# Performance work log

Measured on AMD Instinct MI355X. Metric: run time of the kernel, lower is better.

## Reference

```python
import jax, jax.numpy as jnp
import numpy as np

N_EMBD = 1024
N_HEAD = 16
STRIDE = 128
C = 8
SEQ = 2048
BATCH = 2


def _sparse_causal_mask(nd, ns, stride, c, dtype):
    # Faithful vectorization of _sparse_attention_mask:
    # column j is globally visible if (j % stride) >= stride - c (the last c
    # columns of each stride block), each query also sees its own stride block,
    # and everything is causally masked (j <= q).
    j = jnp.arange(ns)
    q = jnp.arange(ns)[:, None]
    col_sel = (j % stride) >= (stride - c)          # strided summary columns
    same_block = (j[None, :] // stride) == (q // stride)  # local block
    causal = j[None, :] <= q
    mask = ((col_sel[None, :] | same_block) & causal).astype(dtype)
    return mask[ns - nd:]


def setup_inputs() -> dict:
    key = jax.random.key(0)
    k1, k2, k3 = jax.random.split(key, 3)
    inputs = jax.random.normal(k1, (BATCH, SEQ, N_EMBD), dtype=jnp.float32)
    w_attn = jax.random.normal(k2, (N_EMBD, 3 * N_EMBD), dtype=jnp.float32) * 0.02
    b_attn = jnp.zeros((3 * N_EMBD,), dtype=jnp.float32)
    proj_std = 0.02 / np.sqrt(2 * 24)  # n_layer = 24
    w_proj = jax.random.normal(k3, (N_EMBD, N_EMBD), dtype=jnp.float32) * proj_std
    b_proj = jnp.zeros((N_EMBD,), dtype=jnp.float32)
    return {"inputs": inputs, "w_attn": w_attn, "b_attn": b_attn,
            "w_proj": w_proj, "b_proj": b_proj}


def reference(inputs, w_attn, b_attn, w_proj, b_proj):
    B, S, E = inputs.shape
    H = N_HEAD
    D = E // H
    qkv = inputs @ w_attn + b_attn                     # [B,S,3E]
    q, k, v = jnp.split(qkv, 3, axis=-1)
    def split_heads(x):
        return x.reshape(B, S, H, D).transpose(0, 2, 1, 3)  # [B,H,S,D]
    q, k, v = split_heads(q), split_heads(k), split_heads(v)
    present = jnp.stack([k, v], axis=1)                # [B,2,H,S,D]
    scale = jnp.asarray(D, q.dtype) ** 0.5
    w = jnp.einsum('bhqd,bhkd->bhqk', q, k) / scale    # [B,H,S,S]
    mask = _sparse_causal_mask(S, S, STRIDE, C, w.dtype)
    w = w * mask - 1e10 * (1.0 - mask)
    p = jax.nn.softmax(w, axis=-1).astype(v.dtype)
    h = jnp.einsum('bhqk,bhkd->bhqd', p, v)            # [B,H,S,D]
    h = h.transpose(0, 2, 1, 3).reshape(B, S, E)       # merge heads
    h = h @ w_proj + b_proj
    # dropout p=0.0 (eval) -> identity
    return (h, present)
```

## Files before the change

### kernel.cpp

```cpp
#include <hip/hip_runtime.h>
#include <stdint.h>

typedef unsigned short u16;
typedef unsigned int u32;
typedef __attribute__((ext_vector_type(4))) float f32x4;
typedef __attribute__((ext_vector_type(4))) u16 u16x4;
typedef __attribute__((ext_vector_type(8))) __bf16 bf16x8;

__device__ __forceinline__ u16 f2bf(float f) {
  u32 u = __builtin_bit_cast(u32, f);
  u = (u + 0x7FFFu + ((u >> 16) & 1u)) >> 16;
  return (u16)u;
}

__device__ __forceinline__ void gload_lds16(const void* g, void* l) {
  __builtin_amdgcn_global_load_lds(
      (const __attribute__((address_space(1))) void*)(uintptr_t)(g),
      (__attribute__((address_space(3))) void*)(u32)(uintptr_t)(l),
      16, 0, 0);
}

__global__ void k_cvt(const float* __restrict__ in, u16* __restrict__ out, int n4) {
  int i = blockIdx.x * 256 + threadIdx.x;
  if (i >= n4) return;
  f32x4 v = ((const f32x4*)in)[i];
  u16x4 o = { f2bf(v.x), f2bf(v.y), f2bf(v.z), f2bf(v.w) };
  ((u16x4*)out)[i] = o;
}

__global__ void k_transpose(const float* __restrict__ in, u16* __restrict__ out,
                            int K, int N) {
  __shared__ float tile[32][33];
  int n0 = blockIdx.x * 32, k0 = blockIdx.y * 32;
  int t = threadIdx.x;
  int c = t & 31, r0 = t >> 5;
#pragma unroll
  for (int i = 0; i < 4; ++i)
    tile[r0 + i * 8][c] = in[(size_t)(k0 + r0 + i * 8) * N + n0 + c];
  __syncthreads();
  int on = t >> 3, ok = (t & 7) * 4;
  u16x4 o = { f2bf(tile[ok + 0][on]), f2bf(tile[ok + 1][on]),
              f2bf(tile[ok + 2][on]), f2bf(tile[ok + 3][on]) };
  *(u16x4*)&out[(size_t)(n0 + on) * K + k0 + ok] = o;
}

template <int EPI>
__global__ __launch_bounds__(256) void k_gemm(
    const u16* __restrict__ A, const u16* __restrict__ Bt,
    const float* __restrict__ bias, u16* __restrict__ outq,
    float* __restrict__ outp, int M, int N, int K) {
  __shared__ u16 a_lds[128 * 64];
  __shared__ u16 b_lds[128 * 64];
  const int t = threadIdx.x;
  const int lane = t & 63, w = t >> 6;
  const int m0 = blockIdx.y * 128, n0 = blockIdx.x * 128;
  const int srow = t >> 3;
  const int scb = (t & 7) * 16;
  const int ssw = scb ^ ((srow & 7) << 4);
  const size_t pitch = (size_t)K * 2;
  const char* aS = (const char*)A + (size_t)(m0 + srow) * pitch + ssw;
  const char* bS = (const char*)Bt + (size_t)(n0 + srow) * pitch + ssw;
  char* al = (char*)a_lds + t * 16;
  char* bl = (char*)b_lds + t * 16;
  const int wm = (w >> 1) * 64, wn = (w & 1) * 64;
  const int cc = lane & 15, g = lane >> 4;

  f32x4 acc[4][4] = {};

  for (int kt = 0; kt < K; kt += 64) {
    __syncthreads();
#pragma unroll
    for (int i = 0; i < 4; ++i) {
      gload_lds16(aS + (size_t)kt * 2 + (size_t)i * 32 * pitch, al + i * 4096);
      gload_lds16(bS + (size_t)kt * 2 + (size_t)i * 32 * pitch, bl + i * 4096);
    }
    __syncthreads();
#pragma unroll
    for (int kk = 0; kk < 2; ++kk) {
      bf16x8 af[4], bf_[4];
#pragma unroll
      for (int mf = 0; mf < 4; ++mf) {
        int row = wm + mf * 16 + cc;
        af[mf] = *(const bf16x8*)((const char*)a_lds + row * 128 +
                                  ((kk * 64 + g * 16) ^ ((row & 7) << 4)));
      }
#pragma unroll
      for (int nf = 0; nf < 4; ++nf) {
        int row = wn + nf * 16 + cc;
        bf_[nf] = *(const bf16x8*)((const char*)b_lds + row * 128 +
                                   ((kk * 64 + g * 16) ^ ((row & 7) << 4)));
      }
#pragma unroll
      for (int mf = 0; mf < 4; ++mf)
#pragma unroll
        for (int nf = 0; nf < 4; ++nf)
          acc[mf][nf] = __builtin_amdgcn_mfma_f32_16x16x32_bf16(
              af[mf], bf_[nf], acc[mf][nf], 0, 0, 0);
    }
  }

  float bv[4];
#pragma unroll
  for (int nf = 0; nf < 4; ++nf) bv[nf] = bias[n0 + wn + nf * 16 + cc];

#pragma unroll
  for (int mf = 0; mf < 4; ++mf)
#pragma unroll
    for (int nf = 0; nf < 4; ++nf) {
      int n = n0 + wn + nf * 16 + cc;
#pragma unroll
      for (int j = 0; j < 4; ++j) {
        int m = m0 + wm + mf * 16 + g * 4 + j;
        float v = acc[mf][nf][j] + bv[nf];
        if (EPI == 0) {
          if (n < 1024) {
            outq[(size_t)m * 1024 + n] = f2bf(v);
          } else {
            int nn = n - 1024;
            int kv = nn >> 10, n2 = nn & 1023;
            int bb = m >> 11, ss = m & 2047;
            outp[((((size_t)bb * 2 + kv) * 16 + (n2 >> 6)) * 2048 + ss) * 64 +
                 (n2 & 63)] = v;
          }
        } else {
          outp[(size_t)m * N + n] = v;
        }
      }
    }
}

__global__ __launch_bounds__(256) void k_attn(const u16* __restrict__ qws,
                                              const float* __restrict__ present,
                                              u16* __restrict__ hws) {
  const int qb = blockIdx.x, h = blockIdx.y, b = blockIdx.z;
  const int t = threadIdx.x, lane = t & 63, w = t >> 6;
  const int cc = lane & 15, g = lane >> 4;

  __shared__ u16 k_lds[256 * 72];
  __shared__ u16 q_lds[128 * 72];
  __shared__ u16 vt_lds[64 * 264];
  __shared__ u16 p_lds[4][32 * 136];
  __shared__ float rsum[4][32];

  const float* kbase = present + ((size_t)(b * 2 + 0) * 16 + h) * (2048 * 64);
  const float* vbase = present + ((size_t)(b * 2 + 1) * 16 + h) * (2048 * 64);

  {
    int seg = t & 15;
#pragma unroll
    for (int iter = 0; iter < 16; ++iter) {
      int r = (t >> 4) + iter * 16;
      int idx = r - 128;
      int gr = (r < 128) ? (qb * 128 + r) : ((idx >> 3) * 128 + 120 + (idx & 7));
      f32x4 v = *(const f32x4*)(kbase + (size_t)gr * 64 + seg * 4);
      u16x4 o = { f2bf(v.x), f2bf(v.y), f2bf(v.z), f2bf(v.w) };
      *(u16x4*)&k_lds[r * 72 + seg * 4] = o;
    }
  }
  {
    int seg = t & 15;
    int d0 = seg * 4;
#pragma unroll
    for (int iter = 0; iter < 4; ++iter) {
      int r0 = ((t >> 4) + iter * 16) * 4;
      f32x4 vv[4];
#pragma unroll
      for (int i = 0; i < 4; ++i) {
        int r = r0 + i;
        int idx = r - 128;
        int gr = (r < 128) ? (qb * 128 + r) : ((idx >> 3) * 128 + 120 + (idx & 7));
        vv[i] = *(const f32x4*)(vbase + (size_t)gr * 64 + d0);
      }
#pragma unroll
      for (int jd = 0; jd < 4; ++jd) {
        u16x4 o = { f2bf(vv[0][jd]), f2bf(vv[1][jd]),
                    f2bf(vv[2][jd]), f2bf(vv[3][jd]) };
        *(u16x4*)&vt_lds[(d0 + jd) * 264 + r0] = o;
      }
    }
  }
  {
    const char* qsrc = (const char*)qws +
        ((size_t)(b * 2048 + qb * 128 + (t >> 3)) * 1024 + (size_t)h * 64) * 2 +
        (t & 7) * 16;
#pragma unroll
    for (int iter = 0; iter < 4; ++iter) {
      int row = (t >> 3) + iter * 32;
      bf16x8 qv = *(const bf16x8*)(qsrc + (size_t)iter * 32 * 2048);
      *(bf16x8*)((char*)q_lds + row * 144 + (t & 7) * 16) = qv;
    }
  }
  __syncthreads();

  bf16x8 qf_[2][2];
#pragma unroll
  for (int qf = 0; qf < 2; ++qf)
#pragma unroll
    for (int kk = 0; kk < 2; ++kk)
      qf_[qf][kk] = *(const bf16x8*)((const char*)q_lds +
                                     (w * 32 + qf * 16 + cc) * 144 + kk * 64 + g * 16);

  f32x4 s[16][2] = {};
#pragma unroll
  for (int kf = 0; kf < 16; ++kf)
#pragma unroll
    for (int kk = 0; kk < 2; ++kk) {
      bf16x8 kfr = *(const bf16x8*)((const char*)k_lds +
                                    (kf * 16 + cc) * 144 + kk * 64 + g * 16);
#pragma unroll
      for (int qf = 0; qf < 2; ++qf)
        s[kf][qf] = __builtin_amdgcn_mfma_f32_16x16x32_bf16(kfr, qf_[qf][kk],
                                                            s[kf][qf], 0, 0, 0);
    }

  const int nsum = 128 + 8 * qb;
#pragma unroll
  for (int qf = 0; qf < 2; ++qf) {
    int q_local = w * 32 + qf * 16 + cc;
    float mx = -1e30f;
#pragma unroll
    for (int kf = 0; kf < 16; ++kf)
#pragma unroll
      for (int j = 0; j < 4; ++j) {
        int key = kf * 16 + g * 4 + j;
        float v = s[kf][qf][j] * 0.125f;
        bool vis = (key < 128) ? (key <= q_local) : (key < nsum);
        v = vis ? v : -1e30f;
        s[kf][qf][j] = v;
        mx = fmaxf(mx, v);
      }
    mx = fmaxf(mx, __shfl_xor(mx, 16));
    mx = fmaxf(mx, __shfl_xor(mx, 32));
    float sum = 0.f;
#pragma unroll
    for (int kf = 0; kf < 16; ++kf)
#pragma unroll
      for (int j = 0; j < 4; ++j) {
        float p = exp2f((s[kf][qf][j] - mx) * 1.44269504088896f);
        s[kf][qf][j] = p;
        sum += p;
      }
    sum += __shfl_xor(sum, 16);
    sum += __shfl_xor(sum, 32);
    if (g == 0) rsum[w][qf * 16 + cc] = sum;
  }

  f32x4 o_[2][4] = {};
#pragma unroll
  for (int ch = 0; ch < 2; ++ch) {
#pragma unroll
    for (int qf = 0; qf < 2; ++qf)
#pragma unroll
      for (int kf2 = 0; kf2 < 8; ++kf2) {
        int kf = ch * 8 + kf2;
        u16x4 o = { f2bf(s[kf][qf][0]), f2bf(s[kf][qf][1]),
                    f2bf(s[kf][qf][2]), f2bf(s[kf][qf][3]) };
        *(u16x4*)&p_lds[w][(qf * 16 + cc) * 136 + kf2 * 16 + g * 4] = o;
      }
#pragma unroll
    for (int kk = 0; kk < 4; ++kk) {
      bf16x8 pa[2], vb[4];
#pragma unroll
      for (int mf = 0; mf < 2; ++mf)
        pa[mf] = *(const bf16x8*)((const char*)p_lds[w] +
                                  (mf * 16 + cc) * 272 + kk * 64 + g * 16);
#pragma unroll
      for (int nf = 0; nf < 4; ++nf)
        vb[nf] = *(const bf16x8*)((const char*)vt_lds +
                                  (nf * 16 + cc) * 528 + (ch * 4 + kk) * 64 + g * 16);
#pragma unroll
      for (int mf = 0; mf < 2; ++mf)
#pragma unroll
        for (int nf = 0; nf < 4; ++nf)
          o_[mf][nf] = __builtin_amdgcn_mfma_f32_16x16x32_bf16(pa[mf], vb[nf],
                                                               o_[mf][nf], 0, 0, 0);
    }
  }

#pragma unroll
  for (int mf = 0; mf < 2; ++mf)
#pragma unroll
    for (int j = 0; j < 4; ++j) {
      float inv = 1.0f / rsum[w][mf * 16 + g * 4 + j];
      size_t row = (size_t)(b * 2048 + qb * 128 + w * 32 + mf * 16 + g * 4 + j);
#pragma unroll
      for (int nf = 0; nf < 4; ++nf)
        hws[row * 1024 + h * 64 + nf * 16 + cc] = f2bf(o_[mf][nf][j] * inv);
    }
}

extern "C" void kernel_launch(void* const* d_in, const int* in_sizes, int n_in,
                              void* d_out, int out_size, void* d_ws, size_t ws_size,
                              hipStream_t stream) {
  const float* x      = (const float*)d_in[0];
  const float* w_attn = (const float*)d_in[1];
  const float* b_attn = (const float*)d_in[2];
  const float* w_proj = (const float*)d_in[3];
  const float* b_proj = (const float*)d_in[4];
  float* h_out   = (float*)d_out;
  float* present = (float*)d_out + 4194304;

  char* ws = (char*)d_ws;
  u16* xbf = (u16*)(ws);
  u16* qws = (u16*)(ws + (8u << 20));
  u16* wat = (u16*)(ws + (16u << 20));
  u16* wpt = (u16*)(ws + (22u << 20));
  u16* hws = xbf;

  k_cvt<<<4096, 256, 0, stream>>>(x, xbf, 4096 * 1024 / 4);
  k_transpose<<<dim3(96, 32), 256, 0, stream>>>(w_attn, wat, 1024, 3072);
  k_transpose<<<dim3(32, 32), 256, 0, stream>>>(w_proj, wpt, 1024, 1024);
  k_gemm<0><<<dim3(24, 32), 256, 0, stream>>>(xbf, wat, b_attn, qws, present,
                                              4096, 3072, 1024);
  k_attn<<<dim3(16, 16, 2), 256, 0, stream>>>(qws, present, hws);
  k_gemm<1><<<dim3(8, 32), 256, 0, stream>>>(hws, wpt, b_proj, nullptr, h_out,
                                             4096, 1024, 1024);
}
```

Measured before the change: 98.54 us.

## Emit bf16 K and transposed V from QKV GEMM; attention reads directly from global

```diff
diff --git a/kernel.cpp b/kernel.cpp
--- a/kernel.cpp
+++ b/kernel.cpp
@@ -48,7 +48,8 @@
 __global__ __launch_bounds__(256) void k_gemm(
     const u16* __restrict__ A, const u16* __restrict__ Bt,
     const float* __restrict__ bias, u16* __restrict__ outq,
-    float* __restrict__ outp, int M, int N, int K) {
+    float* __restrict__ outp, u16* __restrict__ kbf, u16* __restrict__ vtw,
+    int M, int N, int K) {
   __shared__ u16 a_lds[128 * 64];
   __shared__ u16 b_lds[128 * 64];
   const int t = threadIdx.x;
@@ -108,112 +109,80 @@
 #pragma unroll
     for (int nf = 0; nf < 4; ++nf) {
       int n = n0 + wn + nf * 16 + cc;
-#pragma unroll
-      for (int j = 0; j < 4; ++j) {
-        int m = m0 + wm + mf * 16 + g * 4 + j;
-        float v = acc[mf][nf][j] + bv[nf];
-        if (EPI == 0) {
-          if (n < 1024) {
-            outq[(size_t)m * 1024 + n] = f2bf(v);
-          } else {
-            int nn = n - 1024;
-            int kv = nn >> 10, n2 = nn & 1023;
-            int bb = m >> 11, ss = m & 2047;
-            outp[((((size_t)bb * 2 + kv) * 16 + (n2 >> 6)) * 2048 + ss) * 64 +
-                 (n2 & 63)] = v;
-          }
-        } else {
-          outp[(size_t)m * N + n] = v;
-        }
-      }
-    }
-}
-
-__global__ __launch_bounds__(256) void k_attn(const u16* __restrict__ qws,
-                                              const float* __restrict__ present,
-                                              u16* __restrict__ hws) {
+      int mb = m0 + wm + mf * 16 + g * 4;
+      float v[4];
+#pragma unroll
+      for (int j = 0; j < 4; ++j) v[j] = acc[mf][nf][j] + bv[nf];
+      if (EPI == 1) {
+#pragma unroll
+        for (int j = 0; j < 4; ++j) outp[(size_t)(mb + j) * N + n] = v[j];
+      } else if (n < 1024) {
+#pragma unroll
+        for (int j = 0; j < 4; ++j) outq[(size_t)(mb + j) * 1024 + n] = f2bf(v[j]);
+      } else if (n < 2048) {
+        int n2 = n - 1024, hh = n2 >> 6, d = n2 & 63;
+        int bb = mb >> 11, ss = mb & 2047;
+        float* pr = outp + ((((size_t)bb * 2 + 0) * 16 + hh) * 2048 + ss) * 64 + d;
+        u16* kr = kbf + (((size_t)bb * 16 + hh) * 2048 + ss) * 64 + d;
+#pragma unroll
+        for (int j = 0; j < 4; ++j) { pr[(size_t)j * 64] = v[j]; kr[(size_t)j * 64] = f2bf(v[j]); }
+      } else {
+        int n2 = n - 2048, hh = n2 >> 6, d = n2 & 63;
+        int bb = mb >> 11, ss = mb & 2047;
+        float* pr = outp + ((((size_t)bb * 2 + 1) * 16 + hh) * 2048 + ss) * 64 + d;
+#pragma unroll
+        for (int j = 0; j < 4; ++j) pr[(size_t)j * 64] = v[j];
+        u16x4 o = { f2bf(v[0]), f2bf(v[1]), f2bf(v[2]), f2bf(v[3]) };
+        *(u16x4*)(vtw + (((size_t)bb * 16 + hh) * 64 + d) * 2048 + ss) = o;
+      }
+    }
+}
+
+__global__ __launch_bounds__(256, 2) void k_attn(
+    const u16* __restrict__ qws, const u16* __restrict__ kbf,
+    const u16* __restrict__ vtw, u16* __restrict__ hws) {
   const int qb = blockIdx.x, h = blockIdx.y, b = blockIdx.z;
   const int t = threadIdx.x, lane = t & 63, w = t >> 6;
   const int cc = lane & 15, g = lane >> 4;
 
-  __shared__ u16 k_lds[256 * 72];
-  __shared__ u16 q_lds[128 * 72];
-  __shared__ u16 vt_lds[64 * 264];
   __shared__ u16 p_lds[4][32 * 136];
   __shared__ float rsum[4][32];
 
-  const float* kbase = present + ((size_t)(b * 2 + 0) * 16 + h) * (2048 * 64);
-  const float* vbase = present + ((size_t)(b * 2 + 1) * 16 + h) * (2048 * 64);
-
-  {
-    int seg = t & 15;
-#pragma unroll
-    for (int iter = 0; iter < 16; ++iter) {
-      int r = (t >> 4) + iter * 16;
-      int idx = r - 128;
-      int gr = (r < 128) ? (qb * 128 + r) : ((idx >> 3) * 128 + 120 + (idx & 7));
-      f32x4 v = *(const f32x4*)(kbase + (size_t)gr * 64 + seg * 4);
-      u16x4 o = { f2bf(v.x), f2bf(v.y), f2bf(v.z), f2bf(v.w) };
-      *(u16x4*)&k_lds[r * 72 + seg * 4] = o;
-    }
-  }
-  {
-    int seg = t & 15;
-    int d0 = seg * 4;
-#pragma unroll
-    for (int iter = 0; iter < 4; ++iter) {
-      int r0 = ((t >> 4) + iter * 16) * 4;
-      f32x4 vv[4];
-#pragma unroll
-      for (int i = 0; i < 4; ++i) {
-        int r = r0 + i;
-        int idx = r - 128;
-        int gr = (r < 128) ? (qb * 128 + r) : ((idx >> 3) * 128 + 120 + (idx & 7));
-        vv[i] = *(const f32x4*)(vbase + (size_t)gr * 64 + d0);
-      }
-#pragma unroll
-      for (int jd = 0; jd < 4; ++jd) {
-        u16x4 o = { f2bf(vv[0][jd]), f2bf(vv[1][jd]),
-                    f2bf(vv[2][jd]), f2bf(vv[3][jd]) };
-        *(u16x4*)&vt_lds[(d0 + jd) * 264 + r0] = o;
-      }
-    }
-  }
+  const char* kh = (const char*)kbf + (size_t)(b * 16 + h) * (2048 * 128);
+  const char* vh = (const char*)vtw + (size_t)(b * 16 + h) * (64 * 4096);
+
+  bf16x8 qf_[2][2];
   {
     const char* qsrc = (const char*)qws +
-        ((size_t)(b * 2048 + qb * 128 + (t >> 3)) * 1024 + (size_t)h * 64) * 2 +
-        (t & 7) * 16;
-#pragma unroll
-    for (int iter = 0; iter < 4; ++iter) {
-      int row = (t >> 3) + iter * 32;
-      bf16x8 qv = *(const bf16x8*)(qsrc + (size_t)iter * 32 * 2048);
-      *(bf16x8*)((char*)q_lds + row * 144 + (t & 7) * 16) = qv;
-    }
-  }
-  __syncthreads();
-
-  bf16x8 qf_[2][2];
-#pragma unroll
-  for (int qf = 0; qf < 2; ++qf)
-#pragma unroll
-    for (int kk = 0; kk < 2; ++kk)
-      qf_[qf][kk] = *(const bf16x8*)((const char*)q_lds +
-                                     (w * 32 + qf * 16 + cc) * 144 + kk * 64 + g * 16);
+        (size_t)(b * 2048 + qb * 128 + w * 32 + cc) * 2048 + h * 128 + g * 16;
+#pragma unroll
+    for (int qf = 0; qf < 2; ++qf)
+#pragma unroll
+      for (int kk = 0; kk < 2; ++kk)
+        qf_[qf][kk] = *(const bf16x8*)(qsrc + (size_t)qf * 16 * 2048 + kk * 64);
+  }
+
+  const int nsum = 8 * qb;
+  const int nkf = 8 + ((nsum + 15) >> 4);
 
   f32x4 s[16][2] = {};
 #pragma unroll
-  for (int kf = 0; kf < 16; ++kf)
-#pragma unroll
-    for (int kk = 0; kk < 2; ++kk) {
-      bf16x8 kfr = *(const bf16x8*)((const char*)k_lds +
-                                    (kf * 16 + cc) * 144 + kk * 64 + g * 16);
-#pragma unroll
-      for (int qf = 0; qf < 2; ++qf)
-        s[kf][qf] = __builtin_amdgcn_mfma_f32_16x16x32_bf16(kfr, qf_[qf][kk],
-                                                            s[kf][qf], 0, 0, 0);
-    }
-
-  const int nsum = 128 + 8 * qb;
+  for (int kf = 0; kf < 16; ++kf) {
+    if (kf < nkf) {
+      int row = (kf < 8) ? (qb * 128 + kf * 16 + cc)
+                         : (((kf - 8) * 2 + (cc >> 3)) * 128 + 120 + (cc & 7));
+      const char* kr = kh + (size_t)row * 128 + g * 16;
+#pragma unroll
+      for (int kk = 0; kk < 2; ++kk) {
+        bf16x8 kfr = *(const bf16x8*)(kr + kk * 64);
+#pragma unroll
+        for (int qf = 0; qf < 2; ++qf)
+          s[kf][qf] = __builtin_amdgcn_mfma_f32_16x16x32_bf16(kfr, qf_[qf][kk],
+                                                              s[kf][qf], 0, 0, 0);
+      }
+    }
+  }
+
 #pragma unroll
   for (int qf = 0; qf < 2; ++qf) {
     int q_local = w * 32 + qf * 16 + cc;
@@ -224,7 +193,7 @@
       for (int j = 0; j < 4; ++j) {
         int key = kf * 16 + g * 4 + j;
         float v = s[kf][qf][j] * 0.125f;
-        bool vis = (key < 128) ? (key <= q_local) : (key < nsum);
+        bool vis = (key < 128) ? (key <= q_local) : (key - 128 < nsum);
         v = vis ? v : -1e30f;
         s[kf][qf][j] = v;
         mx = fmaxf(mx, v);
@@ -265,9 +234,12 @@
         pa[mf] = *(const bf16x8*)((const char*)p_lds[w] +
                                   (mf * 16 + cc) * 272 + kk * 64 + g * 16);
 #pragma unroll
-      for (int nf = 0; nf < 4; ++nf)
-        vb[nf] = *(const bf16x8*)((const char*)vt_lds +
-                                  (nf * 16 + cc) * 528 + (ch * 4 + kk) * 64 + g * 16);
+      for (int nf = 0; nf < 4; ++nf) {
+        const char* vrow = vh + (size_t)(nf * 16 + cc) * 4096;
+        int cb = (ch == 0) ? (qb * 256 + kk * 64 + g * 16)
+                           : (((kk * 4 + g) * 128 + 120) * 2);
+        vb[nf] = *(const bf16x8*)(vrow + cb);
+      }
 #pragma unroll
       for (int mf = 0; mf < 2; ++mf)
 #pragma unroll
@@ -305,14 +277,16 @@
   u16* qws = (u16*)(ws + (8u << 20));
   u16* wat = (u16*)(ws + (16u << 20));
   u16* wpt = (u16*)(ws + (22u << 20));
+  u16* kbf = (u16*)(ws + (24u << 20));
+  u16* vtw = (u16*)(ws + (32u << 20));
   u16* hws = xbf;
 
   k_cvt<<<4096, 256, 0, stream>>>(x, xbf, 4096 * 1024 / 4);
   k_transpose<<<dim3(96, 32), 256, 0, stream>>>(w_attn, wat, 1024, 3072);
   k_transpose<<<dim3(32, 32), 256, 0, stream>>>(w_proj, wpt, 1024, 1024);
   k_gemm<0><<<dim3(24, 32), 256, 0, stream>>>(xbf, wat, b_attn, qws, present,
-                                              4096, 3072, 1024);
-  k_attn<<<dim3(16, 16, 2), 256, 0, stream>>>(qws, present, hws);
+                                              kbf, vtw, 4096, 3072, 1024);
+  k_attn<<<dim3(16, 16, 2), 256, 0, stream>>>(qws, kbf, vtw, hws);
   k_gemm<1><<<dim3(8, 32), 256, 0, stream>>>(hws, wpt, b_proj, nullptr, h_out,
-                                             4096, 1024, 1024);
-}
+                                             nullptr, nullptr, 4096, 1024, 1024);
+}
```

Result: slower. 113.3 us (+15.0%).
